# Performance work log

Hardware: AMD Instinct MI355X
Metric: run time of the kernel (lower is better)

Reference implementation:

```python
import jax, jax.numpy as jnp
import numpy as np

B, L, D = 64, 512, 128  # batch, word_len, dim


def setup_inputs() -> dict:
    key = jax.random.key(0)
    ks = jax.random.split(key, 12)
    p = lambda k, s: jax.random.normal(k, s, dtype=jnp.float32) * 0.05
    return {
        "EW": jax.random.normal(ks[0], (B, L, D), dtype=jnp.float32),
        "ES": jax.random.normal(ks[1], (B, L, D), dtype=jnp.float32),
        "WQ_w": p(ks[2], (D, D)), "WQ_b": p(ks[3], (D,)),
        "WK_w": p(ks[4], (D, D)), "WK_b": p(ks[5], (D,)),
        "UQ_w": p(ks[6], (D, D)), "UQ_b": p(ks[7], (D,)),
        "UK_w": p(ks[8], (D, D)), "UK_b": p(ks[9], (D,)),
        "V_w": p(ks[10], (D, D)), "V_b": p(ks[11], (D,)),
    }


def reference(EW, ES, WQ_w, WQ_b, WK_w, WK_b, UQ_w, UQ_b, UK_w, UK_b, V_w, V_b):
    dim = EW.shape[-1]
    word_len = EW.shape[-2]
    scale = 1.0 / (2.0 * dim ** 0.5)
    # word-level Q/K and sentence-level UQ/UK projections (torch Linear: x @ W.T + b)
    Q = (EW @ WQ_w.T + WQ_b) * scale   # [B, L, D]
    K = (EW @ WK_w.T + WK_b) * scale   # [B, L, D]
    UQ = (ES @ UQ_w.T + UQ_b) * scale  # [B, L, D]
    UK = (ES @ UK_w.T + UK_b) * scale  # [B, L, D]
    # two-term score matrix [B, L, L]
    alpha = jnp.einsum('bid,bjd->bij', Q, K) + jnp.einsum('bid,bjd->bij', UQ, UK)
    # manual exp/sum softmax exactly as in the source (no max subtraction;
    # denominator is broadcast along axis 1, faithful to unsqueeze(1))
    numerator = jnp.exp(alpha)                      # [B, L, L]
    denominator = numerator.sum(axis=-1)[:, None, :]  # [B, 1, L]
    soft = numerator / denominator                  # [B, L, L]
    value = EW @ V_w.T + V_b                        # [B, L, D]
    # faithful reinterpreting view (NOT a transpose): [B, L, D] -> [B, D, L]
    value = value.reshape(-1, dim, word_len)
    result = value @ soft                           # [B, D, L]
    return result.reshape(-1, word_len, dim)        # [B, L, D]
```

## Files before the change

### kernel.cpp

```cpp
#include <hip/hip_runtime.h>
#include <hip/hip_bf16.h>

#define NB 64
#define NL 512
#define ND 128
#define NK 256

typedef unsigned short ush;
typedef __attribute__((ext_vector_type(8))) short short8;
typedef __attribute__((ext_vector_type(16))) float f32x16;


__device__ __forceinline__ ush f2bs(float f) {
    union { __hip_bfloat16 h; ush u; } cv;
    cv.h = __float2bfloat16(f);
    return cv.u;
}
__device__ __forceinline__ short8 pack_bf8(float4 a, float4 b) {
    short8 r;
    r[0] = (short)f2bs(a.x); r[1] = (short)f2bs(a.y);
    r[2] = (short)f2bs(a.z); r[3] = (short)f2bs(a.w);
    r[4] = (short)f2bs(b.x); r[5] = (short)f2bs(b.y);
    r[6] = (short)f2bs(b.z); r[7] = (short)f2bs(b.w);
    return r;
}
__device__ __forceinline__ f32x16 zero16() {
    f32x16 z = {0.f,0.f,0.f,0.f,0.f,0.f,0.f,0.f,0.f,0.f,0.f,0.f,0.f,0.f,0.f,0.f};
    return z;
}

__global__ __launch_bounds__(256) void wconv_kernel(
    const float* __restrict__ W0, const float* __restrict__ W1,
    const float* __restrict__ W2, const float* __restrict__ W3,
    const float* __restrict__ W4, ush* __restrict__ Wb)
{
    const int m = blockIdx.y;
    const float* W = (m == 0) ? W0 : (m == 1) ? W1 : (m == 2) ? W2 : (m == 3) ? W3 : W4;
    const int e = (blockIdx.x * 256 + threadIdx.x) * 4;
    float4 v = *(const float4*)(W + e);
    ushort4 o;
    o.x = f2bs(v.x); o.y = f2bs(v.y); o.z = f2bs(v.z); o.w = f2bs(v.w);
    *(ushort4*)(Wb + m * 16384 + e) = o;
}

__global__ __launch_bounds__(256) void projqk_kernel(
    const float* __restrict__ EW, const float* __restrict__ ES,
    const ush* __restrict__ Wb,
    const float* __restrict__ b0, const float* __restrict__ b1,
    const float* __restrict__ b2, const float* __restrict__ b3,
    ush* __restrict__ QUf, ush* __restrict__ KUf)
{
    __shared__ ush Tls[4][2048];
    const int f = blockIdx.x;
    const int xcd = f & 7, loc = f >> 3;
    const int rt = xcd * 32 + (loc >> 2);
    const int m  = loc & 3;
    const int tid = threadIdx.x, w = tid >> 6, lane = tid & 63;
    const int l5 = lane & 31, hi = lane >> 5;
    const float* X = (m >= 2) ? ES : EW;
    const int rbase = rt * 128 + w * 32;

    const float* xr = X + (size_t)(rbase + l5) * ND + hi * 8;
    short8 af[8];
    #pragma unroll
    for (int ks = 0; ks < 8; ++ks)
        af[ks] = pack_bf8(*(const float4*)(xr + ks * 16),
                          *(const float4*)(xr + ks * 16 + 4));

    const ush* Wm = Wb + m * 16384;
    const float* Bp = (m == 0) ? b0 : (m == 1) ? b1 : (m == 2) ? b2 : b3;
    const float scl = 0.044194173824159216f;

    char* Tc = (char*)Tls[w];
    ush* dstf = (m == 0 || m == 2) ? QUf : KUf;
    const int ko = (m >= 2) ? 8 : 0;
    const int p_g = rt * 4 + w;

    #pragma unroll
    for (int pass = 0; pass < 2; ++pass) {
        f32x16 acc[2];
        acc[0] = zero16(); acc[1] = zero16();
        #pragma unroll
        for (int ks = 0; ks < 8; ++ks) {
            #pragma unroll
            for (int nbl = 0; nbl < 2; ++nbl) {
                const int nb = pass * 2 + nbl;
                short8 bf_ = *(const short8*)(Wm + (nb * 32 + l5) * 128 + ks * 16 + hi * 8);
                acc[nbl] = __builtin_amdgcn_mfma_f32_32x32x16_bf16(af[ks], bf_, acc[nbl], 0, 0, 0);
            }
        }
        #pragma unroll
        for (int nbl = 0; nbl < 2; ++nbl) {
            const int nb = pass * 2 + nbl;
            float bias = Bp[nb * 32 + l5];
            #pragma unroll
            for (int r6 = 0; r6 < 16; ++r6) {
                int row = (r6 & 3) + 8 * (r6 >> 2) + 4 * hi;
                int boff = row * 128 + (((nbl * 32 + l5) * 2) ^ ((row & 7) << 4));
                *(ush*)(Tc + boff) = f2bs((acc[nbl][r6] + bias) * scl);
            }
        }
        #pragma unroll
        for (int ks8 = 0; ks8 < 4; ++ks8) {
            int boff = l5 * 128 + ((ks8 * 32 + hi * 16) ^ ((l5 & 7) << 4));
            short8 v = *(const short8*)(Tc + boff);
            int ksg = ko + pass * 4 + ks8;
            *(short8*)(dstf + ((size_t)(p_g * 16 + ksg) * 64 + lane) * 8) = v;
        }
    }
}

__global__ __launch_bounds__(256) void projv_kernel(
    const float* __restrict__ EW, const ush* __restrict__ Wb,
    const float* __restrict__ b4, ush* __restrict__ Vbf)
{
    __shared__ ush lds[16384];
    const int f = blockIdx.x;
    const int rt = (f & 7) * 32 + (f >> 3);
    const int tid = threadIdx.x, w = tid >> 6, lane = tid & 63;
    const int l5 = lane & 31, hi = lane >> 5;
    const int rbase = rt * 128 + w * 32;

    const float* xr = EW + (size_t)(rbase + l5) * ND + hi * 8;
    short8 af[8];
    #pragma unroll
    for (int ks = 0; ks < 8; ++ks)
        af[ks] = pack_bf8(*(const float4*)(xr + ks * 16),
                          *(const float4*)(xr + ks * 16 + 4));

    const ush* Wm = Wb + 4 * 16384;
    f32x16 acc[4];
    acc[0] = zero16(); acc[1] = zero16(); acc[2] = zero16(); acc[3] = zero16();
    #pragma unroll
    for (int ks = 0; ks < 8; ++ks) {
        #pragma unroll
        for (int nb = 0; nb < 4; ++nb) {
            short8 bf_ = *(const short8*)(Wm + (nb * 32 + l5) * 128 + ks * 16 + hi * 8);
            acc[nb] = __builtin_amdgcn_mfma_f32_32x32x16_bf16(af[ks], bf_, acc[nb], 0, 0, 0);
        }
    }

    char* Lc = (char*)lds;
    #pragma unroll
    for (int nb = 0; nb < 4; ++nb) {
        float bias = b4[nb * 32 + l5];
        #pragma unroll
        for (int r6 = 0; r6 < 16; ++r6) {
            int row5 = (r6 & 3) + 8 * (r6 >> 2) + 4 * hi;
            int dl = w * 8 + (row5 >> 2);
            int lcol = (row5 & 3) * 128 + nb * 32 + l5;
            int boff = dl * 1024 + ((lcol * 2) ^ ((dl & 7) << 4));
            *(ush*)(Lc + boff) = f2bs(acc[nb][r6] + bias);
        }
    }
    __syncthreads();
    #pragma unroll
    for (int it = 0; it < 8; ++it) {
        int chunk = it * 256 + tid;
        int ks = chunk >> 6, ln = chunk & 63;
        int l5b = ln & 31, hib = ln >> 5;
        int boff = l5b * 1024 + ((ks * 32 + hib * 16) ^ ((l5b & 7) << 4));
        short8 v = *(const short8*)(Lc + boff);
        *(short8*)(Vbf + ((size_t)(rt * 32 + ks) * 64 + ln) * 8) = v;
    }
}

__global__ __launch_bounds__(256) void alpha_kernel(
    const ush* __restrict__ QUf, const ush* __restrict__ KUf,
    ush* __restrict__ Nf, float* __restrict__ dPart)
{
    __shared__ float red[4][2][16];
    __shared__ ush TlsA[4][2048];
    const int f = blockIdx.x;
    const int xcd = f & 7, loc = f >> 3;
    const int b  = xcd * 8 + (loc >> 5);
    const int rt = (loc >> 1) & 15;
    const int ch = loc & 1;
    const int tid = threadIdx.x, w = tid >> 6, lane = tid & 63;
    const int l5 = lane & 31, hi = lane >> 5;
    const ush* Qb = QUf + (size_t)b * 131072;
    const ush* Kb = KUf + (size_t)b * 131072;
    ush* Nfb = Nf + (size_t)b * 262144;

    const ush* qp = Qb + (size_t)rt * 8192 + lane * 8;
    const int cpg0 = ch * 8 + w * 2;

    f32x16 a0[2], a1[2];
    a0[0] = zero16(); a0[1] = zero16(); a1[0] = zero16(); a1[1] = zero16();
    #pragma unroll
    for (int ks = 0; ks < 16; ks += 2) {
        short8 aqa = *(const short8*)(qp + ks * 512);
        short8 aqb = *(const short8*)(qp + (ks + 1) * 512);
        #pragma unroll
        for (int cp = 0; cp < 2; ++cp) {
            const ush* kp = Kb + (size_t)((cpg0 + cp) * 16) * 512 + lane * 8;
            a0[cp] = __builtin_amdgcn_mfma_f32_32x32x16_bf16(aqa,
                         *(const short8*)(kp + ks * 512), a0[cp], 0, 0, 0);
            a1[cp] = __builtin_amdgcn_mfma_f32_32x32x16_bf16(aqb,
                         *(const short8*)(kp + (ks + 1) * 512), a1[cp], 0, 0, 0);
        }
    }

    float rs[16];
    #pragma unroll
    for (int r6 = 0; r6 < 16; ++r6) rs[r6] = 0.f;
    char* Tc = (char*)TlsA[w];
    #pragma unroll
    for (int cp = 0; cp < 2; ++cp) {
        const int cpg = cpg0 + cp;
        float e[16];
        #pragma unroll
        for (int r6 = 0; r6 < 16; ++r6) {
            e[r6] = __expf(a0[cp][r6] + a1[cp][r6]);
            rs[r6] += e[r6];
        }
        #pragma unroll
        for (int q = 0; q < 8; ++q) {
            int r6 = q * 2;
            int r = (r6 & 3) + 8 * (r6 >> 2) + 4 * hi;
            unsigned int pk = (unsigned int)f2bs(e[r6])
                            | ((unsigned int)f2bs(e[r6 + 1]) << 16);
            *(unsigned int*)(Tc + l5 * 128 + ((r * 2) ^ ((l5 & 7) << 4))) = pk;
        }
        #pragma unroll
        for (int ksl = 0; ksl < 2; ++ksl) {
            short8 v = *(const short8*)(Tc + l5 * 128 +
                           (((ksl * 16 + hi * 8) * 2) ^ ((l5 & 7) << 4)));
            int ksg = rt * 2 + ksl;
            *(short8*)(Nfb + ((size_t)(cpg * 32 + ksg) * 64 + lane) * 8) = v;
        }
    }

    #pragma unroll
    for (int mk = 1; mk <= 16; mk <<= 1)
        #pragma unroll
        for (int r6 = 0; r6 < 16; ++r6) rs[r6] += __shfl_xor(rs[r6], mk, 32);
    if (l5 == 0)
        #pragma unroll
        for (int r6 = 0; r6 < 16; ++r6) red[w][hi][r6] = rs[r6];
    __syncthreads();
    if (tid < 32) {
        int t = tid;
        int hh = (t >> 2) & 1, r6 = (t & 3) + 4 * (t >> 3);
        float s = red[0][hh][r6] + red[1][hh][r6] + red[2][hh][r6] + red[3][hh][r6];
        dPart[((size_t)b * 2 + ch) * NL + rt * 32 + t] = s;
    }
}

__global__ __launch_bounds__(256) void pv_kernel(
    const ush* __restrict__ Vbf, const ush* __restrict__ Nf,
    const float* __restrict__ dPart, float* __restrict__ out)
{
    const int f = blockIdx.x;
    const int xcd = f & 7, loc = f >> 3;
    const int b  = xcd * 8 + (loc >> 4);
    const int ct = loc & 15;
    const int tid = threadIdx.x, w = tid >> 6, lane = tid & 63;
    const int l5 = lane & 31, hi = lane >> 5;
    const ush* Vbb = Vbf + (size_t)b * 65536;
    const ush* Nfb = Nf + (size_t)b * 262144;
    const size_t obase = (size_t)b * (ND * NL);

    const ush* vp = Vbb + (size_t)w * 16384 + lane * 8;
    const ush* np = Nfb + (size_t)ct * 16384 + lane * 8;

    f32x16 acc0 = zero16(), acc1 = zero16();
    #pragma unroll
    for (int ks = 0; ks < 32; ks += 2) {
        acc0 = __builtin_amdgcn_mfma_f32_32x32x16_bf16(*(const short8*)(vp + ks * 512),
                   *(const short8*)(np + ks * 512), acc0, 0, 0, 0);
        acc1 = __builtin_amdgcn_mfma_f32_32x32x16_bf16(*(const short8*)(vp + (ks + 1) * 512),
                   *(const short8*)(np + (ks + 1) * 512), acc1, 0, 0, 0);
    }
    f32x16 acc = acc0 + acc1;
    const int c0 = ct * 32;
    float rd = 1.0f / (dPart[((size_t)b * 2 + 0) * NL + c0 + l5]
                     + dPart[((size_t)b * 2 + 1) * NL + c0 + l5]);
    #pragma unroll
    for (int r6 = 0; r6 < 16; ++r6) {
        int d = w * 32 + (r6 & 3) + 8 * (r6 >> 2) + 4 * hi;
        out[obase + (size_t)d * NL + c0 + l5] = acc[r6] * rd;
    }
}

__global__ __launch_bounds__(256) void fused_kernel(
    const ush* __restrict__ QUf, const ush* __restrict__ KUf,
    const ush* __restrict__ Vbf, float* __restrict__ out)
{
    __shared__ ush Pt[32 * 136];
    __shared__ float red[128];
    __shared__ float rdenS[32];
    const int f = blockIdx.x;
    const int xcd = f & 7, loc = f >> 3;
    const int b  = xcd * 8 + (loc >> 4);
    const int ct = loc & 15, c0 = ct * 32;
    const int tid = threadIdx.x, w = tid >> 6, lane = tid & 63;
    const int l5 = lane & 31, hi = lane >> 5;
    const ush* Qb  = QUf + (size_t)b * 131072;
    const ush* Kb  = KUf + (size_t)b * 131072;
    const ush* Vbb = Vbf + (size_t)b * 65536;
    const size_t obase = (size_t)b * (ND * NL);

    {
        short8 aq[16];
        const ush* qp = Qb + (size_t)ct * 8192 + lane * 8;
        #pragma unroll
        for (int ks = 0; ks < 16; ++ks) aq[ks] = *(const short8*)(qp + ks * 512);
        float rs[16];
        #pragma unroll
        for (int r = 0; r < 16; ++r) rs[r] = 0.f;
        #pragma unroll
        for (int t = 0; t < 4; ++t) {
            const ush* kp = Kb + (size_t)(w * 4 + t) * 8192 + lane * 8;
            f32x16 a0 = zero16(), a1 = zero16();
            #pragma unroll
            for (int ks = 0; ks < 16; ks += 2) {
                a0 = __builtin_amdgcn_mfma_f32_32x32x16_bf16(aq[ks],     *(const short8*)(kp + ks * 512),       a0, 0, 0, 0);
                a1 = __builtin_amdgcn_mfma_f32_32x32x16_bf16(aq[ks + 1], *(const short8*)(kp + (ks + 1) * 512), a1, 0, 0, 0);
            }
            #pragma unroll
            for (int r = 0; r < 16; ++r) rs[r] += __expf(a0[r] + a1[r]);
        }
        #pragma unroll
        for (int mk = 1; mk <= 16; mk <<= 1)
            #pragma unroll
            for (int r = 0; r < 16; ++r) rs[r] += __shfl_xor(rs[r], mk, 32);
        if (l5 == 0)
            #pragma unroll
            for (int r = 0; r < 16; ++r) red[(w * 2 + hi) * 16 + r] = rs[r];
    }
    __syncthreads();
    if (tid < 32) {
        int c = tid;
        int h2 = (c >> 2) & 1, r = (c & 3) + 4 * (c >> 3);
        float s = 0.f;
        #pragma unroll
        for (int kh = 0; kh < 4; ++kh) s += red[(kh * 2 + h2) * 16 + r];
        rdenS[c] = 1.0f / s;
    }
    __syncthreads();

    const int p2 = w;
    const float rden = rdenS[l5];
    const ush* kp2 = Kb + (size_t)ct * 8192 + lane * 8;
    f32x16 oA = zero16(), oB = zero16();

    for (int it = 0; it < 4; ++it) {
        if (it) __syncthreads();
        const ush* qp2 = Qb + (size_t)(it * 4 + p2) * 8192 + lane * 8;
        f32x16 s0 = zero16(), s1 = zero16();
        #pragma unroll
        for (int ks = 0; ks < 16; ks += 2) {
            s0 = __builtin_amdgcn_mfma_f32_32x32x16_bf16(*(const short8*)(qp2 + ks * 512),
                                                         *(const short8*)(kp2 + ks * 512),       s0, 0, 0, 0);
            s1 = __builtin_amdgcn_mfma_f32_32x32x16_bf16(*(const short8*)(qp2 + (ks + 1) * 512),
                                                         *(const short8*)(kp2 + (ks + 1) * 512), s1, 0, 0, 0);
        }
        #pragma unroll
        for (int q = 0; q < 4; ++q) {
            ushort4 pv;
            pv.x = f2bs(__expf(s0[q * 4 + 0] + s1[q * 4 + 0]) * rden);
            pv.y = f2bs(__expf(s0[q * 4 + 1] + s1[q * 4 + 1]) * rden);
            pv.z = f2bs(__expf(s0[q * 4 + 2] + s1[q * 4 + 2]) * rden);
            pv.w = f2bs(__expf(s0[q * 4 + 3] + s1[q * 4 + 3]) * rden);
            int boff = l5 * 272 + (((p2 * 32 + q * 8 + hi * 4) * 2) ^ ((l5 & 7) << 4));
            *(ushort4*)((char*)Pt + boff) = pv;
        }
        __syncthreads();
        #pragma unroll
        for (int j = 0; j < 8; j += 2) {
            short8 va0 = *(const short8*)(Vbb + ((size_t)(p2 * 32 + it * 8 + j) * 64 + lane) * 8);
            short8 pb0 = *(const short8*)((char*)Pt + l5 * 272 + (((j * 16 + hi * 8) * 2) ^ ((l5 & 7) << 4)));
            oA = __builtin_amdgcn_mfma_f32_32x32x16_bf16(va0, pb0, oA, 0, 0, 0);
            short8 va1 = *(const short8*)(Vbb + ((size_t)(p2 * 32 + it * 8 + j + 1) * 64 + lane) * 8);
            short8 pb1 = *(const short8*)((char*)Pt + l5 * 272 + ((((j + 1) * 16 + hi * 8) * 2) ^ ((l5 & 7) << 4)));
            oB = __builtin_amdgcn_mfma_f32_32x32x16_bf16(va1, pb1, oB, 0, 0, 0);
        }
    }
    f32x16 oacc = oA + oB;
    #pragma unroll
    for (int r = 0; r < 16; ++r) {
        int d = p2 * 32 + (r & 3) + 8 * (r >> 2) + 4 * hi;
        out[obase + (size_t)d * NL + c0 + l5] = oacc[r];
    }
}

extern "C" void kernel_launch(void* const* d_in, const int* in_sizes, int n_in,
                              void* d_out, int out_size, void* d_ws, size_t ws_size,
                              hipStream_t stream)
{
    const float* EW   = (const float*)d_in[0];
    const float* ES   = (const float*)d_in[1];
    const float* WQ_w = (const float*)d_in[2];
    const float* WQ_b = (const float*)d_in[3];
    const float* WK_w = (const float*)d_in[4];
    const float* WK_b = (const float*)d_in[5];
    const float* UQ_w = (const float*)d_in[6];
    const float* UQ_b = (const float*)d_in[7];
    const float* UK_w = (const float*)d_in[8];
    const float* UK_b = (const float*)d_in[9];
    const float* V_w  = (const float*)d_in[10];
    const float* V_b  = (const float*)d_in[11];

    if (ws_size < (size_t)41 * 1024 * 1024) return;

    char* ws = (char*)d_ws;
    ush* QUf = (ush*)ws;
    ush* KUf = (ush*)(ws + (size_t)16 * 1024 * 1024);
    ush* Vbf = (ush*)(ws + (size_t)32 * 1024 * 1024);
    ush* Wb  = (ush*)(ws + (size_t)40 * 1024 * 1024);
    float* dPart = (float*)(ws + (size_t)40 * 1024 * 1024 + 512 * 1024);
    ush* Nf  = (ush*)(ws + (size_t)41 * 1024 * 1024);
    float* outp = (float*)d_out;

    wconv_kernel<<<dim3(16, 5), 256, 0, stream>>>(WQ_w, WK_w, UQ_w, UK_w, V_w, Wb);
    projqk_kernel<<<1024, 256, 0, stream>>>(EW, ES, Wb,
                                            WQ_b, WK_b, UQ_b, UK_b, QUf, KUf);
    projv_kernel<<<256, 256, 0, stream>>>(EW, Wb, V_b, Vbf);
    if (ws_size >= (size_t)74 * 1024 * 1024) {
        alpha_kernel<<<2048, 256, 0, stream>>>(QUf, KUf, Nf, dPart);
        pv_kernel<<<1024, 256, 0, stream>>>(Vbf, Nf, dPart, outp);
    } else {
        fused_kernel<<<1024, 256, 0, stream>>>(QUf, KUf, Vbf, outp);
    }
}
```

Before: 80.94 us.

## Fuse alpha and PV stages into one cooperative kernel with grid sync

Replaces the separate alpha and PV kernels with a single cooperative kernel. Each block computes its exp-score tile into shared memory, atomically accumulates column sums into a zeroed global buffer, waits at a grid-wide barrier, then multiplies V by the tile kept in shared memory. This removes the bf16 score matrix round trip through global memory and one kernel launch. In exchange it adds a memset, atomics and a grid barrier, and needs all 1024 blocks co-resident; if the cooperative launch fails it falls back to the old two-kernel path.

```diff
diff --git a/kernel.cpp b/kernel.cpp
--- a/kernel.cpp
+++ b/kernel.cpp
@@ -1,5 +1,6 @@
 #include <hip/hip_runtime.h>
 #include <hip/hip_bf16.h>
+#include <hip/hip_cooperative_groups.h>
 
 #define NB 64
 #define NL 512
@@ -162,6 +163,83 @@
         int boff = l5b * 1024 + ((ks * 32 + hib * 16) ^ ((l5b & 7) << 4));
         short8 v = *(const short8*)(Lc + boff);
         *(short8*)(Vbf + ((size_t)(rt * 32 + ks) * 64 + ln) * 8) = v;
+    }
+}
+
+#define PT_PITCH 1088
+__global__ __launch_bounds__(256, 4) void coop_kernel(
+    const ush* __restrict__ QUf, const ush* __restrict__ KUf,
+    const ush* __restrict__ Vbf, float* __restrict__ dAcc,
+    float* __restrict__ out)
+{
+    __shared__ char Pt[32 * PT_PITCH];
+    const int f = blockIdx.x;
+    const int xcd = f & 7, loc = f >> 3;
+    const int b  = xcd * 8 + (loc >> 4);
+    const int ct = loc & 15, c0 = ct * 32;
+    const int tid = threadIdx.x, w = tid >> 6, lane = tid & 63;
+    const int l5 = lane & 31, hi = lane >> 5;
+    const ush* Qb  = QUf + (size_t)b * 131072;
+    const ush* Kb  = KUf + (size_t)b * 131072;
+    const ush* Vbb = Vbf + (size_t)b * 65536;
+    const size_t obase = (size_t)b * (ND * NL);
+
+    const ush* kbase = Kb + (size_t)ct * 8192 + lane * 8;
+    #pragma unroll
+    for (int t = 0; t < 4; ++t) {
+        const int base = t * 128 + w * 32;
+        const ush* qp = Qb + (size_t)(t * 4 + w) * 8192 + lane * 8;
+        f32x16 a0 = zero16(), a1 = zero16();
+        #pragma unroll
+        for (int ks = 0; ks < 16; ks += 2) {
+            a0 = __builtin_amdgcn_mfma_f32_32x32x16_bf16(*(const short8*)(qp + ks * 512),
+                     *(const short8*)(kbase + ks * 512), a0, 0, 0, 0);
+            a1 = __builtin_amdgcn_mfma_f32_32x32x16_bf16(*(const short8*)(qp + (ks + 1) * 512),
+                     *(const short8*)(kbase + (ks + 1) * 512), a1, 0, 0, 0);
+        }
+        #pragma unroll
+        for (int q = 0; q < 8; ++q) {
+            int r6 = q * 2;
+            int l = base + (r6 & 3) + 8 * (r6 >> 2) + 4 * hi;
+            float e0 = __expf(a0[r6] + a1[r6]);
+            float e1 = __expf(a0[r6 + 1] + a1[r6 + 1]);
+            unsigned int pk = (unsigned int)f2bs(e0) | ((unsigned int)f2bs(e1) << 16);
+            *(unsigned int*)(Pt + l5 * PT_PITCH + l * 2) = pk;
+        }
+    }
+    __syncthreads();
+
+    {
+        int l = tid * 2;
+        float s0 = 0.f, s1 = 0.f;
+        #pragma unroll 8
+        for (int c = 0; c < 32; ++c) {
+            unsigned int u = *(const unsigned int*)(Pt + c * PT_PITCH + l * 2);
+            union { unsigned int i; float v; } lo, hic;
+            lo.i = u << 16; hic.i = u & 0xFFFF0000u;
+            s0 += lo.v; s1 += hic.v;
+        }
+        atomicAdd(dAcc + b * NL + l, s0);
+        atomicAdd(dAcc + b * NL + l + 1, s1);
+    }
+
+    cooperative_groups::this_grid().sync();
+
+    const float rd = 1.0f / dAcc[b * NL + c0 + l5];
+    f32x16 acc0 = zero16(), acc1 = zero16();
+    const ush* vp = Vbb + (size_t)w * 16384 + lane * 8;
+    #pragma unroll
+    for (int ks = 0; ks < 32; ks += 2) {
+        short8 pb0 = *(const short8*)(Pt + l5 * PT_PITCH + (ks * 16 + hi * 8) * 2);
+        acc0 = __builtin_amdgcn_mfma_f32_32x32x16_bf16(*(const short8*)(vp + ks * 512), pb0, acc0, 0, 0, 0);
+        short8 pb1 = *(const short8*)(Pt + l5 * PT_PITCH + ((ks + 1) * 16 + hi * 8) * 2);
+        acc1 = __builtin_amdgcn_mfma_f32_32x32x16_bf16(*(const short8*)(vp + (ks + 1) * 512), pb1, acc1, 0, 0, 0);
+    }
+    f32x16 acc = acc0 + acc1;
+    #pragma unroll
+    for (int r6 = 0; r6 < 16; ++r6) {
+        int d = w * 32 + (r6 & 3) + 8 * (r6 >> 2) + 4 * hi;
+        out[obase + (size_t)d * NL + c0 + l5] = acc[r6] * rd;
     }
 }
 
@@ -287,7 +365,7 @@
     const ush* __restrict__ QUf, const ush* __restrict__ KUf,
     const ush* __restrict__ Vbf, float* __restrict__ out)
 {
-    __shared__ ush Pt[32 * 136];
+    __shared__ ush Pt2[32 * 136];
     __shared__ float red[128];
     __shared__ float rdenS[32];
     const int f = blockIdx.x;
@@ -364,16 +442,16 @@
             pv.z = f2bs(__expf(s0[q * 4 + 2] + s1[q * 4 + 2]) * rden);
             pv.w = f2bs(__expf(s0[q * 4 + 3] + s1[q * 4 + 3]) * rden);
             int boff = l5 * 272 + (((p2 * 32 + q * 8 + hi * 4) * 2) ^ ((l5 & 7) << 4));
-            *(ushort4*)((char*)Pt + boff) = pv;
+            *(ushort4*)((char*)Pt2 + boff) = pv;
         }
         __syncthreads();
         #pragma unroll
         for (int j = 0; j < 8; j += 2) {
             short8 va0 = *(const short8*)(Vbb + ((size_t)(p2 * 32 + it * 8 + j) * 64 + lane) * 8);
-            short8 pb0 = *(const short8*)((char*)Pt + l5 * 272 + (((j * 16 + hi * 8) * 2) ^ ((l5 & 7) << 4)));
+            short8 pb0 = *(const short8*)((char*)Pt2 + l5 * 272 + (((j * 16 + hi * 8) * 2) ^ ((l5 & 7) << 4)));
             oA = __builtin_amdgcn_mfma_f32_32x32x16_bf16(va0, pb0, oA, 0, 0, 0);
             short8 va1 = *(const short8*)(Vbb + ((size_t)(p2 * 32 + it * 8 + j + 1) * 64 + lane) * 8);
-            short8 pb1 = *(const short8*)((char*)Pt + l5 * 272 + ((((j + 1) * 16 + hi * 8) * 2) ^ ((l5 & 7) << 4)));
+            short8 pb1 = *(const short8*)((char*)Pt2 + l5 * 272 + ((((j + 1) * 16 + hi * 8) * 2) ^ ((l5 & 7) << 4)));
             oB = __builtin_amdgcn_mfma_f32_32x32x16_bf16(va1, pb1, oB, 0, 0, 0);
         }
     }
@@ -409,7 +487,7 @@
     ush* KUf = (ush*)(ws + (size_t)16 * 1024 * 1024);
     ush* Vbf = (ush*)(ws + (size_t)32 * 1024 * 1024);
     ush* Wb  = (ush*)(ws + (size_t)40 * 1024 * 1024);
-    float* dPart = (float*)(ws + (size_t)40 * 1024 * 1024 + 512 * 1024);
+    float* dAcc = (float*)(ws + (size_t)40 * 1024 * 1024 + 512 * 1024);
     ush* Nf  = (ush*)(ws + (size_t)41 * 1024 * 1024);
     float* outp = (float*)d_out;
 
@@ -417,9 +495,18 @@
     projqk_kernel<<<1024, 256, 0, stream>>>(EW, ES, Wb,
                                             WQ_b, WK_b, UQ_b, UK_b, QUf, KUf);
     projv_kernel<<<256, 256, 0, stream>>>(EW, Wb, V_b, Vbf);
+
     if (ws_size >= (size_t)74 * 1024 * 1024) {
-        alpha_kernel<<<2048, 256, 0, stream>>>(QUf, KUf, Nf, dPart);
-        pv_kernel<<<1024, 256, 0, stream>>>(Vbf, Nf, dPart, outp);
+        hipError_t err = hipMemsetAsync(dAcc, 0, (size_t)NB * NL * sizeof(float), stream);
+        if (err == hipSuccess) {
+            void* args[] = { (void*)&QUf, (void*)&KUf, (void*)&Vbf, (void*)&dAcc, (void*)&outp };
+            err = hipLaunchCooperativeKernel((const void*)coop_kernel,
+                                             dim3(1024), dim3(256), args, 0, stream);
+        }
+        if (err != hipSuccess) {
+            alpha_kernel<<<2048, 256, 0, stream>>>(QUf, KUf, Nf, dAcc);
+            pv_kernel<<<1024, 256, 0, stream>>>(Vbf, Nf, dAcc, outp);
+        }
     } else {
         fused_kernel<<<1024, 256, 0, stream>>>(QUf, KUf, Vbf, outp);
     }
```

After: 137.1 us. 69.4% more time.
